# Kernel tuning notes

Hardware: AMD Instinct MI355X
Metric: run time of the kernel (lower is better)

## Reference

```python
import jax, jax.numpy as jnp
import numpy as np

ALPHA = 0.01  # ELU slope from init kwargs


def setup_inputs() -> dict:
    key = jax.random.key(0)
    k1, k2, k3, k4, k5 = jax.random.split(key, 5)
    B, L, D_IN, D_ATT = 8, 2048, 256, 128
    context = jax.random.normal(k1, (B, L, D_IN), dtype=jnp.float32)
    query = jax.random.normal(k2, (B, L, D_IN), dtype=jnp.float32)
    query_mask = jax.random.randint(k3, (B, L), 0, 2, dtype=jnp.int32)
    # Linear(in_size, attention_size, bias=False) weights (stored as [in, out])
    W_in = jax.random.normal(k4, (D_IN, D_ATT), dtype=jnp.float32) * 0.05
    W_mem = jax.random.normal(k5, (D_IN, D_ATT), dtype=jnp.float32) * 0.05
    return {"context": context, "query": query, "W_in": W_in,
            "W_mem": W_mem, "query_mask": query_mask}


def reference(context, query, W_in, W_mem, query_mask):
    # VariationalDropout is identity at inference; Linear -> ELU(alpha=0.01)
    inp = jax.nn.elu(jnp.einsum('bld,df->blf', context, W_in), ALPHA)   # [B, Lc, Datt]
    mem = jax.nn.elu(jnp.einsum('bld,df->blf', query, W_mem), ALPHA)    # [B, Lq, Datt]
    scale = inp.shape[-1] ** 0.5
    logits = jnp.einsum('bcf,bqf->bcq', inp, mem) / scale               # [B, Lc, Lq]
    big = jnp.finfo(logits.dtype).max
    # mask_diag=True: kill diagonal (self) positions
    Lq = logits.shape[-1]
    eye = jnp.eye(Lq, dtype=bool)
    logits = jnp.where(eye[None, :, :], -big, logits)
    # masked_softmax over the query axis using query_mask [B, Lq]
    valid = (query_mask > 0)[:, None, :]                                # [B, 1, Lq]
    logits = jnp.where(valid, logits, -big)
    score = jax.nn.softmax(logits, axis=-1)                             # [B, Lc, Lq]
    return jnp.einsum('bcq,bqd->bcd', score, query)                     # [B, Lc, D_in]
```

## Files before the change

### kernel.cpp

```cpp
#include <hip/hip_runtime.h>
#include <math.h>

typedef short v4s __attribute__((ext_vector_type(4)));
typedef short v8s __attribute__((ext_vector_type(8)));
typedef float v4f __attribute__((ext_vector_type(4)));

#define L2E 1.4426950408889634f
#define INV_SCALE 0.08838834764831845f
#define SCL2 (INV_SCALE * L2E)

static __device__ __forceinline__ short f2bf(float x) {
    union { float f; unsigned u; } c; c.f = x;
    unsigned u = c.u;
    unsigned r = (u + 0x7fffu + ((u >> 16) & 1u)) >> 16;
    return (short)r;
}

typedef __attribute__((address_space(3))) void lds_vt;
typedef __attribute__((address_space(1))) const void gl_vt;
static __device__ __forceinline__ void gload_lds16(const void* g, void* l) {
    __builtin_amdgcn_global_load_lds((gl_vt*)g, (lds_vt*)l, 16, 0, 0);
}

__global__ __launch_bounds__(256) void k_pre(const float* __restrict__ ctx,
                                             const float* __restrict__ qry,
                                             const float* __restrict__ Win,
                                             const float* __restrict__ Wmem,
                                             const int* __restrict__ qmask,
                                             short* __restrict__ Qa,
                                             short* __restrict__ Ka,
                                             short* __restrict__ VaT,
                                             float* __restrict__ maskadd) {
    __shared__ __align__(16) char sbuf[64 * 264 * 2];
    int x = blockIdx.x;
    int tid = threadIdx.x;
    if (x < 1024) {
        short* WtS = (short*)sbuf;
        int msel = x & 255, isel = (x >> 8) & 1, nh = (x >> 9) & 1;
        const float* X = isel ? qry : ctx;
        const float* W = isel ? Wmem : Win;
        short* Y = isel ? Ka : Qa;
#pragma unroll 8
        for (int i = 0; i < 64; ++i) {
            int id = i * 256 + tid;
            int k = id >> 6, fp = id & 63;
            WtS[fp * 264 + k] = f2bf(W[k * 128 + nh * 64 + fp]);
        }
        __syncthreads();

        int w = tid >> 6, lane = tid & 63;
        int ln = lane & 15, qd = lane >> 4;
        int m0 = msel * 64 + w * 16;
        v4f zero = {0.f, 0.f, 0.f, 0.f};
        v4f o[4];
#pragma unroll
        for (int i = 0; i < 4; ++i) o[i] = zero;
#pragma unroll
        for (int kk = 0; kk < 8; ++kk) {
            const float* xp = X + (size_t)(m0 + ln) * 256 + kk * 32 + qd * 8;
            float4 x0 = *(const float4*)xp;
            float4 x1 = *(const float4*)(xp + 4);
            v8s a;
            a[0] = f2bf(x0.x); a[1] = f2bf(x0.y); a[2] = f2bf(x0.z); a[3] = f2bf(x0.w);
            a[4] = f2bf(x1.x); a[5] = f2bf(x1.y); a[6] = f2bf(x1.z); a[7] = f2bf(x1.w);
#pragma unroll
            for (int nt = 0; nt < 4; ++nt) {
                v8s bfr = *(const v8s*)(WtS + (nt * 16 + ln) * 264 + kk * 32 + qd * 8);
                o[nt] = __builtin_amdgcn_mfma_f32_16x16x32_bf16(a, bfr, o[nt], 0, 0, 0);
            }
        }
#pragma unroll
        for (int nt = 0; nt < 4; ++nt) {
#pragma unroll
            for (int r = 0; r < 4; ++r) {
                float v = o[nt][r];
                v = v > 0.f ? v : 0.01f * (__expf(v) - 1.f);
                Y[(size_t)(m0 + qd * 4 + r) * 128 + (nh * 4 + nt) * 16 + ln] = f2bf(v);
            }
        }
    } else {
        float (*tile)[65] = (float(*)[65])sbuf;
        int t = x - 1024;
        int q0 = (t & 31) * 64, d0 = ((t >> 5) & 3) * 64, b = t >> 7;
        int c = tid & 63;
        int r4 = tid >> 6;
#pragma unroll
        for (int i = 0; i < 16; ++i) {
            int r = r4 + i * 4;
            tile[r][c] = qry[(size_t)(b * 2048 + q0 + r) * 256 + d0 + c];
        }
        __syncthreads();
        int g = c >> 3, j = c & 7;
#pragma unroll
        for (int i = 0; i < 16; ++i) {
            int d = r4 + i * 4;
            int cs = ((g ^ (d & 7)) << 3) | j;
            VaT[(size_t)(b * 256 + d0 + d) * 2048 + q0 + cs] = f2bf(tile[c][d]);
        }
        if (d0 == 0 && tid < 64) {
            int qq = b * 2048 + q0 + tid;
            maskadd[qq] = (qmask[qq] > 0) ? 0.f : -__builtin_inff();
        }
    }
}

template<int NSPLIT, bool DIRECT>
__global__ __launch_bounds__(256, 2) void k_attn(const short* __restrict__ Qa,
                                                 const short* __restrict__ Ka,
                                                 const short* __restrict__ VaT,
                                                 const float* __restrict__ maskadd,
                                                 float* __restrict__ Opart,
                                                 float* __restrict__ lpart,
                                                 float* __restrict__ out) {
    __shared__ __align__(16) short VaS[2][256 * 64];
    __shared__ __align__(16) short PS[64 * 72];
    __shared__ float lS[4 * 64];

    const int STEPS = 32 / NSPLIT;
    int blk = blockIdx.x;
    int b = blk & 7;
    int t = blk >> 3;
    int c0 = (t & 31) * 64;
    int sp = t >> 5;
    int kv0 = sp * (2048 / NSPLIT);

    int tid = threadIdx.x;
    int w = tid >> 6, lane = tid & 63, ln = lane & 15, qd = lane >> 4;

    const short* qbase = Qa + (size_t)(b * 2048) * 128;
    const short* kbase = Ka + (size_t)(b * 2048 + kv0 + w * 16 + ln) * 128 + qd * 8;
    const short* vbase = VaT + (size_t)(b * 256) * 2048;
    const float* mbase = maskadd + b * 2048 + kv0 + w * 16 + qd * 4;

    v8s qf[4][4];
#pragma unroll
    for (int ct = 0; ct < 4; ++ct) {
        const short* qp = qbase + (size_t)(c0 + ct * 16 + ln) * 128 + qd * 8;
#pragma unroll
        for (int kk = 0; kk < 4; ++kk) qf[ct][kk] = *(const v8s*)(qp + kk * 32);
    }

    v4f zero = {0.f, 0.f, 0.f, 0.f};
    v4f o[4][4];
#pragma unroll
    for (int i = 0; i < 4; ++i)
#pragma unroll
        for (int j = 0; j < 4; ++j) o[i][j] = zero;
    float lacc[4] = {0.f, 0.f, 0.f, 0.f};

    auto stageV = [&](int q0s, int buf) {
        short* base = &VaS[buf][0] + w * 4096;
#pragma unroll
        for (int j = 0; j < 8; ++j) {
            int U = (w * 8 + j) * 64 + lane;
            int d = U >> 3, cc = U & 7;
            gload_lds16(vbase + (size_t)d * 2048 + q0s + cc * 8,
                        base + j * 512);
        }
    };

    stageV(kv0, 0);

    for (int it = 0; it < STEPS; ++it) {
        int q0 = kv0 + it * 64;
        int pb = it & 1;
        stageV(kv0 + ((it + 1) & (STEPS - 1)) * 64, pb ^ 1);

        v8s kf[4];
        const short* kp = kbase + (size_t)it * (64 * 128);
#pragma unroll
        for (int kk = 0; kk < 4; ++kk) kf[kk] = *(const v8s*)(kp + kk * 32);

        float4 mk = *(const float4*)(mbase + it * 64);
        int kvb = q0 + w * 16 + qd * 4;
#pragma unroll
        for (int ct = 0; ct < 4; ++ct) {
            v4f s = zero;
#pragma unroll
            for (int kk = 0; kk < 4; ++kk)
                s = __builtin_amdgcn_mfma_f32_16x16x32_bf16(kf[kk], qf[ct][kk], s, 0, 0, 0);
            int cg = c0 + ct * 16 + ln;
            v4s pw;
            float ls = 0.f;
#pragma unroll
            for (int r = 0; r < 4; ++r) {
                float v = s[r] * SCL2 + (&mk.x)[r];
                if (kvb + r == cg) v = -__builtin_inff();
                float p = exp2f(v);
                ls += p;
                pw[r] = f2bf(p);
            }
            lacc[ct] += ls;
            *(v4s*)(PS + (ct * 16 + ln) * 72 + w * 16 + qd * 4) = pw;
        }
        __syncthreads();

        const short* vs = &VaS[pb][0];
#pragma unroll
        for (int kk2 = 0; kk2 < 2; ++kk2) {
            v8s pf[4], vf[4];
#pragma unroll
            for (int ct = 0; ct < 4; ++ct)
                pf[ct] = *(const v8s*)(PS + (ct * 16 + ln) * 72 + kk2 * 32 + qd * 8);
#pragma unroll
            for (int dt = 0; dt < 4; ++dt) {
                int d = w * 64 + dt * 16 + ln;
                vf[dt] = *(const v8s*)(vs + d * 64 + (((kk2 * 4 + qd) ^ (ln & 7)) << 3));
            }
#pragma unroll
            for (int ct = 0; ct < 4; ++ct)
#pragma unroll
                for (int dt = 0; dt < 4; ++dt)
                    o[ct][dt] = __builtin_amdgcn_mfma_f32_16x16x32_bf16(pf[ct], vf[dt], o[ct][dt], 0, 0, 0);
        }
        __syncthreads();
    }

#pragma unroll
    for (int ct = 0; ct < 4; ++ct) {
        float v = lacc[ct];
        v += __shfl_xor(v, 16);
        v += __shfl_xor(v, 32);
        if (qd == 0) lS[w * 64 + ct * 16 + ln] = v;
    }
    __syncthreads();

#pragma unroll
    for (int ct = 0; ct < 4; ++ct) {
        float4 l0 = *(const float4*)(lS + 0 * 64 + ct * 16 + qd * 4);
        float4 l1 = *(const float4*)(lS + 1 * 64 + ct * 16 + qd * 4);
        float4 l2 = *(const float4*)(lS + 2 * 64 + ct * 16 + qd * 4);
        float4 l3 = *(const float4*)(lS + 3 * 64 + ct * 16 + qd * 4);
        float lv[4];
#pragma unroll
        for (int r = 0; r < 4; ++r)
            lv[r] = (&l0.x)[r] + (&l1.x)[r] + (&l2.x)[r] + (&l3.x)[r];
        int rowg = b * 2048 + c0 + ct * 16 + qd * 4;
        if (DIRECT) {
#pragma unroll
            for (int r = 0; r < 4; ++r) {
                float inv = 1.f / lv[r];
#pragma unroll
                for (int dt = 0; dt < 4; ++dt)
                    out[(size_t)(rowg + r) * 256 + w * 64 + dt * 16 + ln] = o[ct][dt][r] * inv;
            }
        } else {
            float* op = Opart + (size_t)sp * (16384 * 256);
#pragma unroll
            for (int r = 0; r < 4; ++r)
#pragma unroll
                for (int dt = 0; dt < 4; ++dt)
                    op[(size_t)(rowg + r) * 256 + w * 64 + dt * 16 + ln] = o[ct][dt][r];
            if (ln == 0)
                *(float4*)(lpart + sp * 16384 + rowg) = make_float4(lv[0], lv[1], lv[2], lv[3]);
        }
    }
}

template<int NSPLIT>
__global__ __launch_bounds__(256) void k_combine(const float* __restrict__ Opart,
                                                 const float* __restrict__ lpart,
                                                 float* __restrict__ out) {
    int idx = blockIdx.x * 256 + threadIdx.x;
    int row = idx >> 6, d4 = (idx & 63) * 4;
    float L = 0.f;
    float4 acc = {0.f, 0.f, 0.f, 0.f};
#pragma unroll
    for (int s = 0; s < NSPLIT; ++s) {
        L += lpart[s * 16384 + row];
        float4 v = *(const float4*)(Opart + (size_t)s * (16384 * 256) + (size_t)row * 256 + d4);
        acc.x += v.x; acc.y += v.y; acc.z += v.z; acc.w += v.w;
    }
    float inv = 1.f / L;
    float4 res = {acc.x * inv, acc.y * inv, acc.z * inv, acc.w * inv};
    *(float4*)(out + (size_t)row * 256 + d4) = res;
}

extern "C" void kernel_launch(void* const* d_in, const int* in_sizes, int n_in,
                              void* d_out, int out_size, void* d_ws, size_t ws_size,
                              hipStream_t stream) {
    const float* ctx  = (const float*)d_in[0];
    const float* qry  = (const float*)d_in[1];
    const float* win  = (const float*)d_in[2];
    const float* wmem = (const float*)d_in[3];
    const int* qmask  = (const int*)d_in[4];
    float* out = (float*)d_out;

    char* ws = (char*)d_ws;
    short* Qa      = (short*)(ws);
    short* Ka      = (short*)(ws + (4u << 20));
    short* VaT     = (short*)(ws + (8u << 20));
    float* maskadd = (float*)(ws + (16u << 20));
    float* lpart   = (float*)(ws + (16u << 20) + 131072);
    float* Opart   = (float*)(ws + (18u << 20));

    k_pre<<<dim3(2048), 256, 0, stream>>>(ctx, qry, win, wmem, qmask,
                                          Qa, Ka, VaT, maskadd);

    const size_t base = 18u << 20, part = 16u << 20;
    if (ws_size >= base + 2 * part) {
        k_attn<2, false><<<dim3(512), 256, 0, stream>>>(Qa, Ka, VaT, maskadd, Opart, lpart, out);
        k_combine<2><<<dim3(4096), 256, 0, stream>>>(Opart, lpart, out);
    } else {
        k_attn<1, true><<<dim3(256), 256, 0, stream>>>(Qa, Ka, VaT, maskadd, Opart, lpart, out);
    }
}
```

Before: 147.2 us.

## Drop split-KV and LDS V staging; pretranspose weights in separate kernel

Weight transposition to bf16 moves into its own small kernel, and the projection kernel now computes all 128 output features per block by reading weights straight from global memory instead of an LDS copy. The attention kernel loses its two-way KV split and combine pass: 256 blocks each walk the full key range at one block per CU. V fragments are now loaded directly from global memory into registers instead of asynchronously staged into LDS. P is double-buffered so one barrier per iteration is dropped. This removes the partial-output round trip and a kernel launch, but gives up the async prefetch and halves the grid, which may leave CUs idle and expose global latency.

New measurement: 160.6 us. 9.1% more time.

```diff
diff --git a/kernel.cpp b/kernel.cpp
--- a/kernel.cpp
+++ b/kernel.cpp
@@ -16,71 +16,74 @@
     return (short)r;
 }
 
-typedef __attribute__((address_space(3))) void lds_vt;
-typedef __attribute__((address_space(1))) const void gl_vt;
-static __device__ __forceinline__ void gload_lds16(const void* g, void* l) {
-    __builtin_amdgcn_global_load_lds((gl_vt*)g, (lds_vt*)l, 16, 0, 0);
-}
-
-__global__ __launch_bounds__(256) void k_pre(const float* __restrict__ ctx,
-                                             const float* __restrict__ qry,
-                                             const float* __restrict__ Win,
-                                             const float* __restrict__ Wmem,
-                                             const int* __restrict__ qmask,
-                                             short* __restrict__ Qa,
-                                             short* __restrict__ Ka,
-                                             short* __restrict__ VaT,
-                                             float* __restrict__ maskadd) {
-    __shared__ __align__(16) char sbuf[64 * 264 * 2];
+__global__ __launch_bounds__(256) void k_wt(const float* __restrict__ Win,
+                                            const float* __restrict__ Wmem,
+                                            short* __restrict__ WtIn,
+                                            short* __restrict__ WtMem) {
+    const float* W = blockIdx.y ? Wmem : Win;
+    short* Wt = blockIdx.y ? WtMem : WtIn;
+    int id0 = blockIdx.x * 1024;
+#pragma unroll
+    for (int i = 0; i < 4; ++i) {
+        int id = id0 + i * 256 + threadIdx.x;
+        int f = id >> 8, k = id & 255;
+        Wt[id] = f2bf(W[k * 128 + f]);
+    }
+}
+
+__global__ __launch_bounds__(256) void k_main(const float* __restrict__ ctx,
+                                              const float* __restrict__ qry,
+                                              const short* __restrict__ WtIn,
+                                              const short* __restrict__ WtMem,
+                                              const int* __restrict__ qmask,
+                                              short* __restrict__ Qa,
+                                              short* __restrict__ Ka,
+                                              short* __restrict__ VaT,
+                                              float* __restrict__ maskadd) {
+    __shared__ float tile[64][65];
     int x = blockIdx.x;
     int tid = threadIdx.x;
-    if (x < 1024) {
-        short* WtS = (short*)sbuf;
-        int msel = x & 255, isel = (x >> 8) & 1, nh = (x >> 9) & 1;
+    if (x < 512) {
+        int msel = x & 255, isel = x >> 8;
         const float* X = isel ? qry : ctx;
-        const float* W = isel ? Wmem : Win;
+        const short* Wt = isel ? WtMem : WtIn;
         short* Y = isel ? Ka : Qa;
-#pragma unroll 8
-        for (int i = 0; i < 64; ++i) {
-            int id = i * 256 + tid;
-            int k = id >> 6, fp = id & 63;
-            WtS[fp * 264 + k] = f2bf(W[k * 128 + nh * 64 + fp]);
-        }
-        __syncthreads();
-
         int w = tid >> 6, lane = tid & 63;
         int ln = lane & 15, qd = lane >> 4;
         int m0 = msel * 64 + w * 16;
-        v4f zero = {0.f, 0.f, 0.f, 0.f};
-        v4f o[4];
-#pragma unroll
-        for (int i = 0; i < 4; ++i) o[i] = zero;
+
+        v8s a[8];
 #pragma unroll
         for (int kk = 0; kk < 8; ++kk) {
             const float* xp = X + (size_t)(m0 + ln) * 256 + kk * 32 + qd * 8;
             float4 x0 = *(const float4*)xp;
             float4 x1 = *(const float4*)(xp + 4);
-            v8s a;
-            a[0] = f2bf(x0.x); a[1] = f2bf(x0.y); a[2] = f2bf(x0.z); a[3] = f2bf(x0.w);
-            a[4] = f2bf(x1.x); a[5] = f2bf(x1.y); a[6] = f2bf(x1.z); a[7] = f2bf(x1.w);
-#pragma unroll
-            for (int nt = 0; nt < 4; ++nt) {
-                v8s bfr = *(const v8s*)(WtS + (nt * 16 + ln) * 264 + kk * 32 + qd * 8);
-                o[nt] = __builtin_amdgcn_mfma_f32_16x16x32_bf16(a, bfr, o[nt], 0, 0, 0);
+            a[kk][0] = f2bf(x0.x); a[kk][1] = f2bf(x0.y);
+            a[kk][2] = f2bf(x0.z); a[kk][3] = f2bf(x0.w);
+            a[kk][4] = f2bf(x1.x); a[kk][5] = f2bf(x1.y);
+            a[kk][6] = f2bf(x1.z); a[kk][7] = f2bf(x1.w);
+        }
+        v4f zero = {0.f, 0.f, 0.f, 0.f};
+        v4f o[8];
+#pragma unroll
+        for (int i = 0; i < 8; ++i) o[i] = zero;
+#pragma unroll
+        for (int kk = 0; kk < 8; ++kk)
+#pragma unroll
+            for (int nt = 0; nt < 8; ++nt) {
+                v8s bfr = *(const v8s*)(Wt + (size_t)(nt * 16 + ln) * 256 + kk * 32 + qd * 8);
+                o[nt] = __builtin_amdgcn_mfma_f32_16x16x32_bf16(a[kk], bfr, o[nt], 0, 0, 0);
             }
-        }
-#pragma unroll
-        for (int nt = 0; nt < 4; ++nt) {
+#pragma unroll
+        for (int nt = 0; nt < 8; ++nt)
 #pragma unroll
             for (int r = 0; r < 4; ++r) {
                 float v = o[nt][r];
                 v = v > 0.f ? v : 0.01f * (__expf(v) - 1.f);
-                Y[(size_t)(m0 + qd * 4 + r) * 128 + (nh * 4 + nt) * 16 + ln] = f2bf(v);
+                Y[(size_t)(m0 + qd * 4 + r) * 128 + nt * 16 + ln] = f2bf(v);
             }
-        }
     } else {
-        float (*tile)[65] = (float(*)[65])sbuf;
-        int t = x - 1024;
+        int t = x - 512;
         int q0 = (t & 31) * 64, d0 = ((t >> 5) & 3) * 64, b = t >> 7;
         int c = tid & 63;
         int r4 = tid >> 6;
@@ -90,12 +93,10 @@
             tile[r][c] = qry[(size_t)(b * 2048 + q0 + r) * 256 + d0 + c];
         }
         __syncthreads();
-        int g = c >> 3, j = c & 7;
 #pragma unroll
         for (int i = 0; i < 16; ++i) {
             int d = r4 + i * 4;
-            int cs = ((g ^ (d & 7)) << 3) | j;
-            VaT[(size_t)(b * 256 + d0 + d) * 2048 + q0 + cs] = f2bf(tile[c][d]);
+            VaT[(size_t)(b * 256 + d0 + d) * 2048 + q0 + c] = f2bf(tile[c][d]);
         }
         if (d0 == 0 && tid < 64) {
             int qq = b * 2048 + q0 + tid;
@@ -104,38 +105,24 @@
     }
 }
 
-template<int NSPLIT, bool DIRECT>
-__global__ __launch_bounds__(256, 2) void k_attn(const short* __restrict__ Qa,
+__global__ __launch_bounds__(256, 1) void k_attn(const short* __restrict__ Qa,
                                                  const short* __restrict__ Ka,
                                                  const short* __restrict__ VaT,
                                                  const float* __restrict__ maskadd,
-                                                 float* __restrict__ Opart,
-                                                 float* __restrict__ lpart,
                                                  float* __restrict__ out) {
-    __shared__ __align__(16) short VaS[2][256 * 64];
-    __shared__ __align__(16) short PS[64 * 72];
-    __shared__ float lS[4 * 64];
-
-    const int STEPS = 32 / NSPLIT;
+    __shared__ __align__(16) short PS[2][64 * 72];
+    __shared__ float lS[4][64];
+
     int blk = blockIdx.x;
     int b = blk & 7;
-    int t = blk >> 3;
-    int c0 = (t & 31) * 64;
-    int sp = t >> 5;
-    int kv0 = sp * (2048 / NSPLIT);
-
+    int c0 = (blk >> 3) * 64;
     int tid = threadIdx.x;
     int w = tid >> 6, lane = tid & 63, ln = lane & 15, qd = lane >> 4;
 
-    const short* qbase = Qa + (size_t)(b * 2048) * 128;
-    const short* kbase = Ka + (size_t)(b * 2048 + kv0 + w * 16 + ln) * 128 + qd * 8;
-    const short* vbase = VaT + (size_t)(b * 256) * 2048;
-    const float* mbase = maskadd + b * 2048 + kv0 + w * 16 + qd * 4;
-
     v8s qf[4][4];
 #pragma unroll
     for (int ct = 0; ct < 4; ++ct) {
-        const short* qp = qbase + (size_t)(c0 + ct * 16 + ln) * 128 + qd * 8;
+        const short* qp = Qa + (size_t)(b * 2048 + c0 + ct * 16 + ln) * 128 + qd * 8;
 #pragma unroll
         for (int kk = 0; kk < 4; ++kk) qf[ct][kk] = *(const v8s*)(qp + kk * 32);
     }
@@ -148,30 +135,25 @@
         for (int j = 0; j < 4; ++j) o[i][j] = zero;
     float lacc[4] = {0.f, 0.f, 0.f, 0.f};
 
-    auto stageV = [&](int q0s, int buf) {
-        short* base = &VaS[buf][0] + w * 4096;
-#pragma unroll
-        for (int j = 0; j < 8; ++j) {
-            int U = (w * 8 + j) * 64 + lane;
-            int d = U >> 3, cc = U & 7;
-            gload_lds16(vbase + (size_t)d * 2048 + q0s + cc * 8,
-                        base + j * 512);
-        }
-    };
-
-    stageV(kv0, 0);
-
-    for (int it = 0; it < STEPS; ++it) {
-        int q0 = kv0 + it * 64;
-        int pb = it & 1;
-        stageV(kv0 + ((it + 1) & (STEPS - 1)) * 64, pb ^ 1);
-
+    const short* kbase = Ka + (size_t)(b * 2048 + w * 16 + ln) * 128 + qd * 8;
+    const short* vbase = VaT + (size_t)(b * 256) * 2048;
+    const float* mbase = maskadd + b * 2048 + w * 16 + qd * 4;
+
+    for (int it = 0; it < 32; ++it) {
+        int q0 = it * 64, pb = it & 1;
         v8s kf[4];
-        const short* kp = kbase + (size_t)it * (64 * 128);
+        const short* kp = kbase + (size_t)q0 * 128;
 #pragma unroll
         for (int kk = 0; kk < 4; ++kk) kf[kk] = *(const v8s*)(kp + kk * 32);
-
-        float4 mk = *(const float4*)(mbase + it * 64);
+        float4 mk = *(const float4*)(mbase + q0);
+        v8s vf[2][4];
+#pragma unroll
+        for (int kk2 = 0; kk2 < 2; ++kk2)
+#pragma unroll
+            for (int dt = 0; dt < 4; ++dt)
+                vf[kk2][dt] = *(const v8s*)(vbase + (size_t)(w * 64 + dt * 16 + ln) * 2048
+                                            + q0 + kk2 * 32 + qd * 8);
+
         int kvb = q0 + w * 16 + qd * 4;
 #pragma unroll
         for (int ct = 0; ct < 4; ++ct) {
@@ -191,29 +173,22 @@
                 pw[r] = f2bf(p);
             }
             lacc[ct] += ls;
-            *(v4s*)(PS + (ct * 16 + ln) * 72 + w * 16 + qd * 4) = pw;
+            *(v4s*)(&PS[pb][(ct * 16 + ln) * 72 + w * 16 + qd * 4]) = pw;
         }
         __syncthreads();
 
-        const short* vs = &VaS[pb][0];
 #pragma unroll
         for (int kk2 = 0; kk2 < 2; ++kk2) {
-            v8s pf[4], vf[4];
+            v8s pf[4];
 #pragma unroll
             for (int ct = 0; ct < 4; ++ct)
-                pf[ct] = *(const v8s*)(PS + (ct * 16 + ln) * 72 + kk2 * 32 + qd * 8);
-#pragma unroll
-            for (int dt = 0; dt < 4; ++dt) {
-                int d = w * 64 + dt * 16 + ln;
-                vf[dt] = *(const v8s*)(vs + d * 64 + (((kk2 * 4 + qd) ^ (ln & 7)) << 3));
-            }
+                pf[ct] = *(const v8s*)(&PS[pb][(ct * 16 + ln) * 72 + kk2 * 32 + qd * 8]);
 #pragma unroll
             for (int ct = 0; ct < 4; ++ct)
 #pragma unroll
                 for (int dt = 0; dt < 4; ++dt)
-                    o[ct][dt] = __builtin_amdgcn_mfma_f32_16x16x32_bf16(pf[ct], vf[dt], o[ct][dt], 0, 0, 0);
-        }
-        __syncthreads();
+                    o[ct][dt] = __builtin_amdgcn_mfma_f32_16x16x32_bf16(pf[ct], vf[kk2][dt], o[ct][dt], 0, 0, 0);
+        }
     }
 
 #pragma unroll
@@ -221,59 +196,23 @@
         float v = lacc[ct];
         v += __shfl_xor(v, 16);
         v += __shfl_xor(v, 32);
-        if (qd == 0) lS[w * 64 + ct * 16 + ln] = v;
+        if (qd == 0) lS[w][ct * 16 + ln] = v;
     }
     __syncthreads();
 
 #pragma unroll
     for (int ct = 0; ct < 4; ++ct) {
-        float4 l0 = *(const float4*)(lS + 0 * 64 + ct * 16 + qd * 4);
-        float4 l1 = *(const float4*)(lS + 1 * 64 + ct * 16 + qd * 4);
-        float4 l2 = *(const float4*)(lS + 2 * 64 + ct * 16 + qd * 4);
-        float4 l3 = *(const float4*)(lS + 3 * 64 + ct * 16 + qd * 4);
-        float lv[4];
-#pragma unroll
-        for (int r = 0; r < 4; ++r)
-            lv[r] = (&l0.x)[r] + (&l1.x)[r] + (&l2.x)[r] + (&l3.x)[r];
         int rowg = b * 2048 + c0 + ct * 16 + qd * 4;
-        if (DIRECT) {
-#pragma unroll
-            for (int r = 0; r < 4; ++r) {
-                float inv = 1.f / lv[r];
-#pragma unroll
-                for (int dt = 0; dt < 4; ++dt)
-                    out[(size_t)(rowg + r) * 256 + w * 64 + dt * 16 + ln] = o[ct][dt][r] * inv;
-            }
-        } else {
-            float* op = Opart + (size_t)sp * (16384 * 256);
-#pragma unroll
-            for (int r = 0; r < 4; ++r)
-#pragma unroll
-                for (int dt = 0; dt < 4; ++dt)
-                    op[(size_t)(rowg + r) * 256 + w * 64 + dt * 16 + ln] = o[ct][dt][r];
-            if (ln == 0)
-                *(float4*)(lpart + sp * 16384 + rowg) = make_float4(lv[0], lv[1], lv[2], lv[3]);
-        }
-    }
-}
-
-template<int NSPLIT>
-__global__ __launch_bounds__(256) void k_combine(const float* __restrict__ Opart,
-                                                 const float* __restrict__ lpart,
-                                                 float* __restrict__ out) {
-    int idx = blockIdx.x * 256 + threadIdx.x;
-    int row = idx >> 6, d4 = (idx & 63) * 4;
-    float L = 0.f;
-    float4 acc = {0.f, 0.f, 0.f, 0.f};
-#pragma unroll
-    for (int s = 0; s < NSPLIT; ++s) {
-        L += lpart[s * 16384 + row];
-        float4 v = *(const float4*)(Opart + (size_t)s * (16384 * 256) + (size_t)row * 256 + d4);
-        acc.x += v.x; acc.y += v.y; acc.z += v.z; acc.w += v.w;
-    }
-    float inv = 1.f / L;
-    float4 res = {acc.x * inv, acc.y * inv, acc.z * inv, acc.w * inv};
-    *(float4*)(out + (size_t)row * 256 + d4) = res;
+#pragma unroll
+        for (int r = 0; r < 4; ++r) {
+            int ci = ct * 16 + qd * 4 + r;
+            float lv = lS[0][ci] + lS[1][ci] + lS[2][ci] + lS[3][ci];
+            float inv = 1.f / lv;
+#pragma unroll
+            for (int dt = 0; dt < 4; ++dt)
+                out[(size_t)(rowg + r) * 256 + w * 64 + dt * 16 + ln] = o[ct][dt][r] * inv;
+        }
+    }
 }
 
 extern "C" void kernel_launch(void* const* d_in, const int* in_sizes, int n_in,
@@ -291,17 +230,11 @@
     short* Ka      = (short*)(ws + (4u << 20));
     short* VaT     = (short*)(ws + (8u << 20));
     float* maskadd = (float*)(ws + (16u << 20));
-    float* lpart   = (float*)(ws + (16u << 20) + 131072);
-    float* Opart   = (float*)(ws + (18u << 20));
-
-    k_pre<<<dim3(2048), 256, 0, stream>>>(ctx, qry, win, wmem, qmask,
-                                          Qa, Ka, VaT, maskadd);
-
-    const size_t base = 18u << 20, part = 16u << 20;
-    if (ws_size >= base + 2 * part) {
-        k_attn<2, false><<<dim3(512), 256, 0, stream>>>(Qa, Ka, VaT, maskadd, Opart, lpart, out);
-        k_combine<2><<<dim3(4096), 256, 0, stream>>>(Opart, lpart, out);
-    } else {
-        k_attn<1, true><<<dim3(256), 256, 0, stream>>>(Qa, Ka, VaT, maskadd, Opart, lpart, out);
-    }
-}
+    short* WtIn    = (short*)(ws + (16u << 20) + 65536);
+    short* WtMem   = (short*)(ws + (16u << 20) + 131072);
+
+    k_wt<<<dim3(32, 2), 256, 0, stream>>>(win, wmem, WtIn, WtMem);
+    k_main<<<dim3(1536), 256, 0, stream>>>(ctx, qry, WtIn, WtMem, qmask,
+                                           Qa, Ka, VaT, maskadd);
+    k_attn<<<dim3(256), 256, 0, stream>>>(Qa, Ka, VaT, maskadd, out);
+}
```
